# Optimization experiments

Hardware: AMD Instinct MI355X
Metric: run time of the kernel (lower is better)

## Reference

```python
import jax
import jax.numpy as jnp
import numpy as np
from jax import lax

B, T, D = 32, 256, 512   # batch, seq len, controller_dim (== memory_dim)
S = 2048                 # memory_slots
EPS_LN = 1e-5            # nn.LayerNorm default eps
EPS_NRM = 1e-12          # F.normalize default eps


def setup_inputs() -> dict:
    key = jax.random.key(0)
    ks = jax.random.split(key, 12)
    sc = 1.0 / np.sqrt(D)  # roughly torch Linear init scale
    return {
        "controller_seq": jax.random.normal(ks[0], (B, T, D), dtype=jnp.float32),
        "memory": jax.random.normal(ks[1], (S, D), dtype=jnp.float32),
        "Wk": jax.random.normal(ks[2], (D, D), dtype=jnp.float32) * sc,
        "bk": jax.random.normal(ks[3], (D,), dtype=jnp.float32) * sc,
        "We": jax.random.normal(ks[4], (D, D), dtype=jnp.float32) * sc,
        "be": jax.random.normal(ks[5], (D,), dtype=jnp.float32) * sc,
        "Ww": jax.random.normal(ks[6], (D, D), dtype=jnp.float32) * sc,
        "bw": jax.random.normal(ks[7], (D,), dtype=jnp.float32) * sc,
        "Wg": jax.random.normal(ks[8], (D, D), dtype=jnp.float32) * sc,
        "bg": jax.random.normal(ks[9], (D,), dtype=jnp.float32) * sc,
        "gamma": jnp.ones((D,), dtype=jnp.float32),
        "beta": jnp.zeros((D,), dtype=jnp.float32),
    }


def _l2norm(x, axis=-1):
    # matches F.normalize: x / max(||x||, eps)
    n = jnp.sqrt(jnp.sum(x * x, axis=axis, keepdims=True))
    return x / jnp.maximum(n, EPS_NRM)


def _layernorm(x, gamma, beta):
    mu = jnp.mean(x, axis=-1, keepdims=True)
    var = jnp.mean((x - mu) ** 2, axis=-1, keepdims=True)
    return (x - mu) * lax.rsqrt(var + EPS_LN) * gamma + beta


def reference(controller_seq, memory, Wk, bk, We, be, Ww, bw, Wg, bg, gamma, beta):
    batch = controller_seq.shape[0]

    def step(mem, c):  # mem: [S, Dm], c: [B, Dc]
        # --- read (addressing by cosine similarity) ---
        k = c @ Wk.T + bk                       # [B, Dm]
        sim = _l2norm(k) @ _l2norm(mem).T       # [B, S]
        w = jax.nn.softmax(sim, axis=-1)        # [B, S]
        read_val = w @ mem                      # [B, Dm]
        # --- write (erase / add, averaged over batch) ---
        erase = jax.nn.sigmoid(c @ We.T + be)   # [B, Dm]
        add = c @ Ww.T + bw                     # [B, Dm]
        # mean_b (1 - w_bs * e_bd) = 1 - (w^T e)/B ; avoids [B,S,Dm] intermediate
        erase_m = 1.0 - jnp.einsum("bs,bd->sd", w, erase) / batch
        add_m = jnp.einsum("bs,bd->sd", w, add) / batch
        new_mem = _layernorm(mem * erase_m + add_m, gamma, beta)  # dropout in eval mode
        # --- gated output ---
        g = jax.nn.sigmoid(c @ Wg.T + bg)       # [B, Dm]
        out_t = g * c + (1.0 - g) * read_val
        return new_mem, out_t

    _, outs = lax.scan(step, memory, jnp.swapaxes(controller_seq, 0, 1))  # outs: [T, B, D]
    return jnp.swapaxes(outs, 0, 1)  # [B, T, D]
```

## Files before the change

kernel.cpp:

```cpp
#include <hip/hip_runtime.h>

#define DEV __device__ __forceinline__

namespace {
constexpr int Bc = 32;
constexpr int Tc = 256;
constexpr int Dc = 512;
constexpr int NBLK = 256;
constexpr int NW   = 128;
constexpr int ROWS = 16;

constexpr size_t OFF_KN   = 0;
constexpr size_t OFF_E    = OFF_KN + (size_t)Tc * Bc * Dc;
constexpr size_t OFF_A    = OFF_E  + (size_t)Tc * Bc * Dc;
constexpr size_t OFF_RP   = OFF_A  + (size_t)Tc * Bc * Dc;
constexpr size_t OFF_DENP = OFF_RP + (size_t)2 * NW * Bc * Dc;
constexpr size_t OFF_FLAGS= OFF_DENP + (size_t)2 * NW * Bc;
constexpr size_t OFF_GO   = OFF_FLAGS + 256 * 16;
}

DEV float sigm(float x) { return 1.0f / (1.0f + __expf(-x)); }

DEV float ld1cg(const float* p) {
  unsigned u = __hip_atomic_load((const unsigned*)p, __ATOMIC_RELAXED,
                                 __HIP_MEMORY_SCOPE_AGENT);
  return __uint_as_float(u);
}
DEV void st1cg(float* p, float v) {
  __hip_atomic_store((unsigned*)p, __float_as_uint(v), __ATOMIC_RELAXED,
                     __HIP_MEMORY_SCOPE_AGENT);
}
DEV float2 ld2cg(const float* p) {
  unsigned long long u = __hip_atomic_load((const unsigned long long*)p,
                                           __ATOMIC_RELAXED, __HIP_MEMORY_SCOPE_AGENT);
  union { unsigned long long u; float2 f; } c; c.u = u; return c.f;
}
DEV void st2cg(float* p, float2 v) {
  union { float2 f; unsigned long long u; } c; c.f = v;
  __hip_atomic_store((unsigned long long*)p, c.u, __ATOMIC_RELAXED,
                     __HIP_MEMORY_SCOPE_AGENT);
}

__global__ __launch_bounds__(256) void k_gemm(
    const float* __restrict__ A,
    const float* __restrict__ Wk, const float* __restrict__ bk,
    const float* __restrict__ We, const float* __restrict__ be,
    const float* __restrict__ Ww, const float* __restrict__ bw,
    const float* __restrict__ Wg, const float* __restrict__ bg,
    float* __restrict__ ws, float* __restrict__ gout)
{
  __shared__ float As[32][68];
  __shared__ float Bs[32][68];

  const int bid = blockIdx.x;
  const int mat = bid >> 10;
  const int rem = bid & 1023;
  const int rt = rem >> 3, jt = rem & 7;
  const int rbase = rt * 64, jbase = jt * 64;

  const float* Wm; const float* bm;
  if      (mat == 0) { Wm = Wk; bm = bk; }
  else if (mat == 1) { Wm = We; bm = be; }
  else if (mat == 2) { Wm = Ww; bm = bw; }
  else               { Wm = Wg; bm = bg; }

  const int tid = threadIdx.x;
  const int lr = tid >> 2;
  const int lk = (tid & 3) * 8;
  const int ty = tid >> 4, tx = tid & 15;

  float acc[4][4] = {};

  for (int k0 = 0; k0 < Dc; k0 += 32) {
    const float4 a0 = *(const float4*)&A [(size_t)(rbase + lr) * Dc + k0 + lk];
    const float4 a1 = *(const float4*)&A [(size_t)(rbase + lr) * Dc + k0 + lk + 4];
    const float4 b0 = *(const float4*)&Wm[(size_t)(jbase + lr) * Dc + k0 + lk];
    const float4 b1 = *(const float4*)&Wm[(size_t)(jbase + lr) * Dc + k0 + lk + 4];
    __syncthreads();
    As[lk + 0][lr] = a0.x; As[lk + 1][lr] = a0.y; As[lk + 2][lr] = a0.z; As[lk + 3][lr] = a0.w;
    As[lk + 4][lr] = a1.x; As[lk + 5][lr] = a1.y; As[lk + 6][lr] = a1.z; As[lk + 7][lr] = a1.w;
    Bs[lk + 0][lr] = b0.x; Bs[lk + 1][lr] = b0.y; Bs[lk + 2][lr] = b0.z; Bs[lk + 3][lr] = b0.w;
    Bs[lk + 4][lr] = b1.x; Bs[lk + 5][lr] = b1.y; Bs[lk + 6][lr] = b1.z; Bs[lk + 7][lr] = b1.w;
    __syncthreads();
    #pragma unroll
    for (int kk = 0; kk < 32; ++kk) {
      const float4 av = *(const float4*)&As[kk][ty * 4];
      const float4 bv = *(const float4*)&Bs[kk][tx * 4];
      const float ar[4] = {av.x, av.y, av.z, av.w};
      const float br[4] = {bv.x, bv.y, bv.z, bv.w};
      #pragma unroll
      for (int i = 0; i < 4; ++i)
        #pragma unroll
        for (int j = 0; j < 4; ++j)
          acc[i][j] = fmaf(ar[i], br[j], acc[i][j]);
    }
  }

  const float4 bias = *(const float4*)&bm[jbase + tx * 4];
  const float bi[4] = {bias.x, bias.y, bias.z, bias.w};
  #pragma unroll
  for (int i = 0; i < 4; ++i) {
    const int r = rbase + ty * 4 + i;
    float v[4];
    #pragma unroll
    for (int j = 0; j < 4; ++j) {
      v[j] = acc[i][j] + bi[j];
      if (mat & 1) v[j] = sigm(v[j]);
    }
    float4 o; o.x = v[0]; o.y = v[1]; o.z = v[2]; o.w = v[3];
    if (mat == 3) {
      *(float4*)&gout[(size_t)r * Dc + jbase + tx * 4] = o;
    } else {
      float* dst = ws + (mat == 0 ? OFF_KN : (mat == 1 ? OFF_E : OFF_A));
      const int t = r & 255, b = r >> 8;
      *(float4*)&dst[((size_t)t * Bc + b) * Dc + jbase + tx * 4] = o;
    }
  }
}

__global__ __launch_bounds__(256) void k_knorm(float* __restrict__ kn)
{
  const int row = blockIdx.x * 4 + (threadIdx.x >> 6);
  const int lane = threadIdx.x & 63;
  float* p = kn + (size_t)row * Dc;
  float4 v0 = *(const float4*)&p[lane * 4];
  float4 v1 = *(const float4*)&p[256 + lane * 4];
  float ss = v0.x*v0.x + v0.y*v0.y + v0.z*v0.z + v0.w*v0.w
           + v1.x*v1.x + v1.y*v1.y + v1.z*v1.z + v1.w*v1.w;
  #pragma unroll
  for (int off = 32; off >= 1; off >>= 1) ss += __shfl_xor(ss, off);
  const float inv = 1.0f / fmaxf(sqrtf(ss), 1e-12f);
  v0.x *= inv; v0.y *= inv; v0.z *= inv; v0.w *= inv;
  v1.x *= inv; v1.y *= inv; v1.z *= inv; v1.w *= inv;
  *(float4*)&p[lane * 4] = v0;
  *(float4*)&p[256 + lane * 4] = v1;
}

DEV void gbar(unsigned* flags, unsigned* go, unsigned step, int bid, int tid)
{
  __syncthreads();
  if (bid == 0) {
    if (tid > 0) {
      while (__hip_atomic_load(&flags[tid * 16], __ATOMIC_RELAXED,
                               __HIP_MEMORY_SCOPE_AGENT) < step)
        __builtin_amdgcn_s_sleep(2);
    }
    __syncthreads();
    if (tid == 0)
      __hip_atomic_store(go, step, __ATOMIC_RELAXED, __HIP_MEMORY_SCOPE_AGENT);
  } else {
    if (tid == 0) {
      __hip_atomic_store(&flags[bid * 16], step, __ATOMIC_RELAXED,
                         __HIP_MEMORY_SCOPE_AGENT);
      while (__hip_atomic_load(go, __ATOMIC_RELAXED,
                               __HIP_MEMORY_SCOPE_AGENT) < step)
        __builtin_amdgcn_s_sleep(2);
    }
    __syncthreads();
  }
}

DEV void sim_phase(const float* __restrict__ knp, float* __restrict__ denp_row,
                   const float (*y)[516], float* __restrict__ ew_own,
                   const float* invn_s, float* sred, int tid)
{
  const int r = tid >> 4, bp = tid & 15;
  const float* k0p = knp + (size_t)bp * Dc;
  const float* k1p = knp + (size_t)(bp + 16) * Dc;
  float acc0 = 0.f, acc1 = 0.f;
  #pragma unroll 4
  for (int dq = 0; dq < Dc / 4; ++dq) {
    const float4 y4 = *(const float4*)&y[r][dq * 4];
    const float4 ka = *(const float4*)&k0p[dq * 4];
    const float4 kb = *(const float4*)&k1p[dq * 4];
    acc0 = fmaf(y4.x, ka.x, acc0); acc0 = fmaf(y4.y, ka.y, acc0);
    acc0 = fmaf(y4.z, ka.z, acc0); acc0 = fmaf(y4.w, ka.w, acc0);
    acc1 = fmaf(y4.x, kb.x, acc1); acc1 = fmaf(y4.y, kb.y, acc1);
    acc1 = fmaf(y4.z, kb.z, acc1); acc1 = fmaf(y4.w, kb.w, acc1);
  }
  const float iv = invn_s[r];
  const float e0 = __expf(acc0 * iv);
  const float e1 = __expf(acc1 * iv);
  ew_own[r * 32 + bp]      = e0;
  ew_own[r * 32 + bp + 16] = e1;
  if (tid < 32) sred[tid] = 0.f;
  __syncthreads();
  atomicAdd(&sred[bp], e0);
  atomicAdd(&sred[bp + 16], e1);
  __syncthreads();
  if (tid < 32) st1cg(&denp_row[tid], sred[tid]);
}

__global__ __launch_bounds__(256) void k_main(
    const float* __restrict__ cs, const float* __restrict__ mem_in,
    const float* __restrict__ gamma, const float* __restrict__ beta,
    float* __restrict__ ws, float* __restrict__ out)
{
  __shared__ float mrows[16][516];
  __shared__ float ew_own[16 * 32];
  __shared__ float wbuf[16][32];
  __shared__ float lds_red[256];
  __shared__ float2 red2[256];
  __shared__ float sred[32];
  __shared__ float mu_s[16], rs_s[16], invn_s[16], dinv_s[32];

  float* kn   = ws + OFF_KN;
  float* eptb = ws + OFF_E;
  float* aptb = ws + OFF_A;
  float* rp   = ws + OFF_RP;
  float* denp = ws + OFF_DENP;
  unsigned* flags = (unsigned*)(ws + OFF_FLAGS);
  unsigned* go    = (unsigned*)(ws + OFF_GO);

  const int bid = blockIdx.x, tid = threadIdx.x;
  const float inv32 = 1.0f / 32.0f;

  if (bid < NW) {
    const int s0 = bid * ROWS;
    const int c0 = tid * 2;
    #pragma unroll
    for (int r = 0; r < ROWS; ++r)
      *(float2*)&mrows[r][c0] = *(const float2*)&mem_in[(size_t)(s0 + r) * Dc + c0];
    __syncthreads();
    {
      const int row = tid >> 4, li = tid & 15;
      float ss = 0.f;
      #pragma unroll
      for (int i = 0; i < 8; ++i) {
        const float4 v = *(const float4*)&mrows[row][(li + i * 16) * 4];
        ss += v.x*v.x + v.y*v.y + v.z*v.z + v.w*v.w;
      }
      ss += __shfl_xor(ss, 8); ss += __shfl_xor(ss, 4);
      ss += __shfl_xor(ss, 2); ss += __shfl_xor(ss, 1);
      if (li == 0) invn_s[row] = 1.0f / fmaxf(sqrtf(ss), 1e-12f);
    }
    __syncthreads();
    sim_phase(kn, denp + (size_t)bid * Bc, mrows, ew_own, invn_s, sred, tid);
  }
  gbar(flags, go, 1u, bid, tid);

  for (int t = 0; t <= Tc; ++t) {
    if (bid < NW) {
      if (t < Tc) {
        const int c0 = tid * 2;
        {
          const float* dp = denp + (size_t)(t & 1) * NW * Bc;
          const int b = tid & 31, ch = tid >> 5;
          float s = 0.f;
          #pragma unroll
          for (int g = 0; g < 16; ++g)
            s += ld1cg(&dp[(size_t)(ch * 16 + g) * Bc + b]);
          lds_red[tid] = s;
          __syncthreads();
          if (tid < 32) {
            float tot = 0.f;
            #pragma unroll
            for (int c2 = 0; c2 < 8; ++c2) tot += lds_red[c2 * 32 + tid];
            dinv_s[tid] = 1.0f / tot;
          }
          __syncthreads();
        }
        for (int idx = tid; idx < ROWS * 32; idx += 256)
          wbuf[idx >> 5][idx & 31] = ew_own[idx] * dinv_s[idx & 31];
        __syncthreads();

        float2 mr[ROWS];
        #pragma unroll
        for (int r = 0; r < ROWS; ++r) mr[r] = *(const float2*)&mrows[r][c0];

        {
          float* rpd = rp + (size_t)(t & 1) * NW * Bc * Dc
                          + (size_t)bid * Bc * Dc + c0;
          #pragma unroll 4
          for (int b = 0; b < 32; ++b) {
            float2 a; a.x = 0.f; a.y = 0.f;
            #pragma unroll
            for (int r = 0; r < ROWS; ++r) {
              const float wv = wbuf[r][b];
              a.x = fmaf(wv, mr[r].x, a.x);
              a.y = fmaf(wv, mr[r].y, a.y);
            }
            st2cg(rpd + (size_t)b * Dc, a);
          }
        }

        if (t < Tc - 1) {
          float2 er[ROWS] = {}, ad[ROWS] = {};
          const float* ept = eptb + (size_t)t * Bc * Dc;
          const float* apt = aptb + (size_t)t * Bc * Dc;
          #pragma unroll 4
          for (int b = 0; b < 32; ++b) {
            const float2 ev = *(const float2*)&ept[(size_t)b * Dc + c0];
            const float2 av = *(const float2*)&apt[(size_t)b * Dc + c0];
            #pragma unroll
            for (int r = 0; r < ROWS; ++r) {
              const float wv = wbuf[r][b];
              er[r].x = fmaf(wv, ev.x, er[r].x); er[r].y = fmaf(wv, ev.y, er[r].y);
              ad[r].x = fmaf(wv, av.x, ad[r].x); ad[r].y = fmaf(wv, av.y, ad[r].y);
            }
          }
          float2 xr[ROWS];
          #pragma unroll
          for (int r = 0; r < ROWS; ++r) {
            float2 x;
            x.x = mr[r].x * (1.0f - er[r].x * inv32) + ad[r].x * inv32;
            x.y = mr[r].y * (1.0f - er[r].y * inv32) + ad[r].y * inv32;
            xr[r] = x;
            *(float2*)&mrows[r][c0] = x;
          }
          __syncthreads();
          {
            const int row = tid >> 4, li = tid & 15;
            float s1 = 0.f, s2 = 0.f;
            #pragma unroll
            for (int i = 0; i < 8; ++i) {
              const float4 v = *(const float4*)&mrows[row][(li + i * 16) * 4];
              s1 += v.x + v.y + v.z + v.w;
              s2 += v.x*v.x + v.y*v.y + v.z*v.z + v.w*v.w;
            }
            s1 += __shfl_xor(s1, 8); s2 += __shfl_xor(s2, 8);
            s1 += __shfl_xor(s1, 4); s2 += __shfl_xor(s2, 4);
            s1 += __shfl_xor(s1, 2); s2 += __shfl_xor(s2, 2);
            s1 += __shfl_xor(s1, 1); s2 += __shfl_xor(s2, 1);
            if (li == 0) {
              const float mu = s1 * (1.0f / 512.0f);
              const float var = s2 * (1.0f / 512.0f) - mu * mu;
              mu_s[row] = mu;
              rs_s[row] = rsqrtf(var + 1e-5f);
            }
          }
          __syncthreads();
          const float2 gm  = *(const float2*)&gamma[c0];
          const float2 bt2 = *(const float2*)&beta[c0];
          #pragma unroll
          for (int r = 0; r < ROWS; ++r) {
            const float mu = mu_s[r], rs = rs_s[r];
            float2 y;
            y.x = (xr[r].x - mu) * rs * gm.x + bt2.x;
            y.y = (xr[r].y - mu) * rs * gm.y + bt2.y;
            *(float2*)&mrows[r][c0] = y;
          }
          __syncthreads();
          {
            const int row = tid >> 4, li = tid & 15;
            float ss = 0.f;
            #pragma unroll
            for (int i = 0; i < 8; ++i) {
              const float4 v = *(const float4*)&mrows[row][(li + i * 16) * 4];
              ss += v.x*v.x + v.y*v.y + v.z*v.z + v.w*v.w;
            }
            ss += __shfl_xor(ss, 8); ss += __shfl_xor(ss, 4);
            ss += __shfl_xor(ss, 2); ss += __shfl_xor(ss, 1);
            if (li == 0) invn_s[row] = 1.0f / fmaxf(sqrtf(ss), 1e-12f);
          }
          __syncthreads();
          sim_phase(kn + (size_t)(t + 1) * Bc * Dc,
                    denp + (size_t)((t + 1) & 1) * NW * Bc + (size_t)bid * Bc,
                    mrows, ew_own, invn_s, sred, tid);
        }
      }
    } else {
      if (t >= 1) {
        const int t0 = t - 1;
        const int rb = bid - NW;
        const int b = rb >> 2;
        const int d0 = (rb & 3) * 128;
        const float* rpc = rp + (size_t)(t0 & 1) * NW * Bc * Dc
                              + (size_t)b * Dc + d0;
        const int jp = (tid & 63) * 2;
        const int q  = tid >> 6;
        float2 a; a.x = 0.f; a.y = 0.f;
        #pragma unroll 4
        for (int pi = 0; pi < 32; ++pi) {
          const int p = q * 32 + pi;
          const float2 v = ld2cg(rpc + (size_t)p * Bc * Dc + jp);
          a.x += v.x; a.y += v.y;
        }
        red2[tid] = a;
        __syncthreads();
        if (tid < 64) {
          const float2 v0 = red2[tid];
          const float2 v1 = red2[64 + tid];
          const float2 v2 = red2[128 + tid];
          const float2 v3 = red2[192 + tid];
          float2 rv;
          rv.x = (v0.x + v1.x) + (v2.x + v3.x);
          rv.y = (v0.y + v1.y) + (v2.y + v3.y);
          const size_t oofs = ((size_t)b * Tc + t0) * Dc + d0 + tid * 2;
          const float2 g  = *(const float2*)&out[oofs];
          const float2 cv = *(const float2*)&cs[oofs];
          float2 o;
          o.x = g.x * cv.x + (1.0f - g.x) * rv.x;
          o.y = g.y * cv.y + (1.0f - g.y) * rv.y;
          *(float2*)&out[oofs] = o;
        }
        __syncthreads();
      }
    }
    if (t < Tc) gbar(flags, go, (unsigned)(t + 2), bid, tid);
  }
}

extern "C" void kernel_launch(void* const* d_in, const int* in_sizes, int n_in,
                              void* d_out, int out_size, void* d_ws, size_t ws_size,
                              hipStream_t stream)
{
  const float* cs    = (const float*)d_in[0];
  const float* mem   = (const float*)d_in[1];
  const float* Wk    = (const float*)d_in[2];
  const float* bk    = (const float*)d_in[3];
  const float* We    = (const float*)d_in[4];
  const float* be    = (const float*)d_in[5];
  const float* Ww    = (const float*)d_in[6];
  const float* bw    = (const float*)d_in[7];
  const float* Wg    = (const float*)d_in[8];
  const float* bg    = (const float*)d_in[9];
  const float* gamma = (const float*)d_in[10];
  const float* beta  = (const float*)d_in[11];
  float* ws  = (float*)d_ws;
  float* out = (float*)d_out;

  hipMemsetAsync(ws + OFF_FLAGS, 0, (256 * 16 + 1) * sizeof(unsigned), stream);

  hipLaunchKernelGGL(k_gemm, dim3(4096), dim3(256), 0, stream,
                     cs, Wk, bk, We, be, Ww, bw, Wg, bg, ws, out);
  hipLaunchKernelGGL(k_knorm, dim3(2048), dim3(256), 0, stream, ws + OFF_KN);
  hipLaunchKernelGGL(k_main, dim3(NBLK), dim3(256), 0, stream,
                     cs, mem, gamma, beta, ws, out);
}
```

Before: 10.66 ms.

## Prefetch next-step keys and erase/add vectors; use all-to-all flag barrier

Replaces the two-level grid barrier, where block 0 gathers flags and broadcasts a go flag, with a flat barrier: each block publishes its flag and each thread polls one block's flag. The memory-row blocks now stage the next timestep's normalized keys into LDS early in the step, and preload the next step's erase/add vectors into registers before the barrier. This moves global-memory latency off the serial per-step critical path. In exchange it uses more LDS and registers (launch bounds set to one block per CU), and every block now polls 256 flags each step.

```diff
diff --git a/kernel.cpp b/kernel.cpp
--- a/kernel.cpp
+++ b/kernel.cpp
@@ -16,7 +16,6 @@
 constexpr size_t OFF_RP   = OFF_A  + (size_t)Tc * Bc * Dc;
 constexpr size_t OFF_DENP = OFF_RP + (size_t)2 * NW * Bc * Dc;
 constexpr size_t OFF_FLAGS= OFF_DENP + (size_t)2 * NW * Bc;
-constexpr size_t OFF_GO   = OFF_FLAGS + 256 * 16;
 }
 
 DEV float sigm(float x) { return 1.0f / (1.0f + __expf(-x)); }
@@ -136,43 +135,29 @@
   *(float4*)&p[256 + lane * 4] = v1;
 }
 
-DEV void gbar(unsigned* flags, unsigned* go, unsigned step, int bid, int tid)
+DEV void gbar(unsigned* flags, unsigned step, int bid, int tid)
 {
   __syncthreads();
-  if (bid == 0) {
-    if (tid > 0) {
-      while (__hip_atomic_load(&flags[tid * 16], __ATOMIC_RELAXED,
-                               __HIP_MEMORY_SCOPE_AGENT) < step)
-        __builtin_amdgcn_s_sleep(2);
-    }
-    __syncthreads();
-    if (tid == 0)
-      __hip_atomic_store(go, step, __ATOMIC_RELAXED, __HIP_MEMORY_SCOPE_AGENT);
-  } else {
-    if (tid == 0) {
-      __hip_atomic_store(&flags[bid * 16], step, __ATOMIC_RELAXED,
-                         __HIP_MEMORY_SCOPE_AGENT);
-      while (__hip_atomic_load(go, __ATOMIC_RELAXED,
-                               __HIP_MEMORY_SCOPE_AGENT) < step)
-        __builtin_amdgcn_s_sleep(2);
-    }
-    __syncthreads();
-  }
-}
-
-DEV void sim_phase(const float* __restrict__ knp, float* __restrict__ denp_row,
+  if (tid == 0)
+    __hip_atomic_store(&flags[bid * 16], step, __ATOMIC_RELAXED,
+                       __HIP_MEMORY_SCOPE_AGENT);
+  while (__hip_atomic_load(&flags[tid * 16], __ATOMIC_RELAXED,
+                           __HIP_MEMORY_SCOPE_AGENT) < step)
+    __builtin_amdgcn_s_sleep(1);
+  __syncthreads();
+}
+
+DEV void sim_phase(const float (*knb)[516], float* __restrict__ denp_row,
                    const float (*y)[516], float* __restrict__ ew_own,
                    const float* invn_s, float* sred, int tid)
 {
   const int r = tid >> 4, bp = tid & 15;
-  const float* k0p = knp + (size_t)bp * Dc;
-  const float* k1p = knp + (size_t)(bp + 16) * Dc;
   float acc0 = 0.f, acc1 = 0.f;
   #pragma unroll 4
   for (int dq = 0; dq < Dc / 4; ++dq) {
     const float4 y4 = *(const float4*)&y[r][dq * 4];
-    const float4 ka = *(const float4*)&k0p[dq * 4];
-    const float4 kb = *(const float4*)&k1p[dq * 4];
+    const float4 ka = *(const float4*)&knb[bp][dq * 4];
+    const float4 kb = *(const float4*)&knb[bp + 16][dq * 4];
     acc0 = fmaf(y4.x, ka.x, acc0); acc0 = fmaf(y4.y, ka.y, acc0);
     acc0 = fmaf(y4.z, ka.z, acc0); acc0 = fmaf(y4.w, ka.w, acc0);
     acc1 = fmaf(y4.x, kb.x, acc1); acc1 = fmaf(y4.y, kb.y, acc1);
@@ -191,12 +176,13 @@
   if (tid < 32) st1cg(&denp_row[tid], sred[tid]);
 }
 
-__global__ __launch_bounds__(256) void k_main(
+__global__ __launch_bounds__(256, 1) void k_main(
     const float* __restrict__ cs, const float* __restrict__ mem_in,
     const float* __restrict__ gamma, const float* __restrict__ beta,
     float* __restrict__ ws, float* __restrict__ out)
 {
   __shared__ float mrows[16][516];
+  __shared__ float knbuf[32][516];
   __shared__ float ew_own[16 * 32];
   __shared__ float wbuf[16][32];
   __shared__ float lds_red[256];
@@ -210,10 +196,11 @@
   float* rp   = ws + OFF_RP;
   float* denp = ws + OFF_DENP;
   unsigned* flags = (unsigned*)(ws + OFF_FLAGS);
-  unsigned* go    = (unsigned*)(ws + OFF_GO);
 
   const int bid = blockIdx.x, tid = threadIdx.x;
   const float inv32 = 1.0f / 32.0f;
+
+  float2 ev[32], av[32];
 
   if (bid < NW) {
     const int s0 = bid * ROWS;
@@ -221,6 +208,17 @@
     #pragma unroll
     for (int r = 0; r < ROWS; ++r)
       *(float2*)&mrows[r][c0] = *(const float2*)&mem_in[(size_t)(s0 + r) * Dc + c0];
+    #pragma unroll
+    for (int i = 0; i < 16; ++i) {
+      const int idx = tid + i * 256;
+      const int row = idx >> 7, col = (idx & 127) * 4;
+      *(float4*)&knbuf[row][col] = *(const float4*)&kn[row * Dc + col];
+    }
+    #pragma unroll
+    for (int b = 0; b < 32; ++b) {
+      ev[b] = *(const float2*)&eptb[(size_t)b * Dc + c0];
+      av[b] = *(const float2*)&aptb[(size_t)b * Dc + c0];
+    }
     __syncthreads();
     {
       const int row = tid >> 4, li = tid & 15;
@@ -235,14 +233,23 @@
       if (li == 0) invn_s[row] = 1.0f / fmaxf(sqrtf(ss), 1e-12f);
     }
     __syncthreads();
-    sim_phase(kn, denp + (size_t)bid * Bc, mrows, ew_own, invn_s, sred, tid);
+    sim_phase(knbuf, denp + (size_t)bid * Bc, mrows, ew_own, invn_s, sred, tid);
   }
-  gbar(flags, go, 1u, bid, tid);
+  gbar(flags, 1u, bid, tid);
 
   for (int t = 0; t <= Tc; ++t) {
     if (bid < NW) {
       if (t < Tc) {
         const int c0 = tid * 2;
+        if (t < Tc - 1) {
+          const float* src = kn + (size_t)(t + 1) * Bc * Dc;
+          #pragma unroll
+          for (int i = 0; i < 16; ++i) {
+            const int idx = tid + i * 256;
+            const int row = idx >> 7, col = (idx & 127) * 4;
+            *(float4*)&knbuf[row][col] = *(const float4*)&src[row * Dc + col];
+          }
+        }
         {
           const float* dp = denp + (size_t)(t & 1) * NW * Bc;
           const int b = tid & 31, ch = tid >> 5;
@@ -267,7 +274,6 @@
         float2 mr[ROWS];
         #pragma unroll
         for (int r = 0; r < ROWS; ++r) mr[r] = *(const float2*)&mrows[r][c0];
-
         {
           float* rpd = rp + (size_t)(t & 1) * NW * Bc * Dc
                           + (size_t)bid * Bc * Dc + c0;
@@ -286,17 +292,14 @@
 
         if (t < Tc - 1) {
           float2 er[ROWS] = {}, ad[ROWS] = {};
-          const float* ept = eptb + (size_t)t * Bc * Dc;
-          const float* apt = aptb + (size_t)t * Bc * Dc;
-          #pragma unroll 4
+          #pragma unroll
           for (int b = 0; b < 32; ++b) {
-            const float2 ev = *(const float2*)&ept[(size_t)b * Dc + c0];
-            const float2 av = *(const float2*)&apt[(size_t)b * Dc + c0];
+            const float2 e2 = ev[b], a2 = av[b];
             #pragma unroll
             for (int r = 0; r < ROWS; ++r) {
               const float wv = wbuf[r][b];
-              er[r].x = fmaf(wv, ev.x, er[r].x); er[r].y = fmaf(wv, ev.y, er[r].y);
-              ad[r].x = fmaf(wv, av.x, ad[r].x); ad[r].y = fmaf(wv, av.y, ad[r].y);
+              er[r].x = fmaf(wv, e2.x, er[r].x); er[r].y = fmaf(wv, e2.y, er[r].y);
+              ad[r].x = fmaf(wv, a2.x, ad[r].x); ad[r].y = fmaf(wv, a2.y, ad[r].y);
             }
           }
           float2 xr[ROWS];
@@ -307,6 +310,15 @@
             x.y = mr[r].y * (1.0f - er[r].y * inv32) + ad[r].y * inv32;
             xr[r] = x;
             *(float2*)&mrows[r][c0] = x;
+          }
+          if (t <= Tc - 3) {
+            const float* ep1 = eptb + (size_t)(t + 1) * Bc * Dc;
+            const float* ap1 = aptb + (size_t)(t + 1) * Bc * Dc;
+            #pragma unroll
+            for (int b = 0; b < 32; ++b) {
+              ev[b] = *(const float2*)&ep1[(size_t)b * Dc + c0];
+              av[b] = *(const float2*)&ap1[(size_t)b * Dc + c0];
+            }
           }
           __syncthreads();
           {
@@ -354,7 +366,7 @@
             if (li == 0) invn_s[row] = 1.0f / fmaxf(sqrtf(ss), 1e-12f);
           }
           __syncthreads();
-          sim_phase(kn + (size_t)(t + 1) * Bc * Dc,
+          sim_phase(knbuf,
                     denp + (size_t)((t + 1) & 1) * NW * Bc + (size_t)bid * Bc,
                     mrows, ew_own, invn_s, sred, tid);
         }
@@ -397,7 +409,7 @@
         __syncthreads();
       }
     }
-    if (t < Tc) gbar(flags, go, (unsigned)(t + 2), bid, tid);
+    if (t < Tc) gbar(flags, (unsigned)(t + 2), bid, tid);
   }
 }
 
@@ -420,7 +432,7 @@
   float* ws  = (float*)d_ws;
   float* out = (float*)d_out;
 
-  hipMemsetAsync(ws + OFF_FLAGS, 0, (256 * 16 + 1) * sizeof(unsigned), stream);
+  hipMemsetAsync(ws + OFF_FLAGS, 0, 256 * 16 * sizeof(unsigned), stream);
 
   hipLaunchKernelGGL(k_gemm, dim3(4096), dim3(256), 0, stream,
                      cs, Wk, bk, We, be, Ww, bw, Wg, bg, ws, out);
```

After: 9.902 ms. 1.08x faster.
